# Optimization experiments

Measured on AMD Instinct MI355X. Metric: run time of the kernel, lower is better.

Reference implementation:

```python
import jax, jax.numpy as jnp
import numpy as np

NUM_SEGMENTS = 4
SIZE_SEG = 2  # sqrt(num_segments)


def conv2d_same(x, w, b):
    # x: [B,C,H,W], w: [O,I,3,3], padding=1, stride=1
    y = jax.lax.conv_general_dilated(
        x, w, window_strides=(1, 1), padding=((1, 1), (1, 1)),
        dimension_numbers=("NCHW", "OIHW", "NCHW"))
    return y + b[None, :, None, None]


def setup_inputs() -> dict:
    key = jax.random.key(0)
    k1, k2, k3, k4, k5 = jax.random.split(key, 5)
    B, C, H, W = 4, 64, 512, 512
    x = jax.random.normal(k1, (B, C, H, W), dtype=jnp.float32)
    # Conv params (kaiming-ish small scale)
    local_w = jax.random.normal(k2, (NUM_SEGMENTS, NUM_SEGMENTS, 3, 3), dtype=jnp.float32) * 0.1
    local_b = jax.random.normal(k3, (NUM_SEGMENTS,), dtype=jnp.float32) * 0.01
    global_w = jax.random.normal(k4, (1, 2, 3, 3), dtype=jnp.float32) * 0.1
    global_b = jax.random.normal(k5, (1,), dtype=jnp.float32) * 0.01
    return {"x": x, "local_w": local_w, "local_b": local_b,
            "global_w": global_w, "global_b": global_b}


def local_attention(x, w, b):
    B, C, H, W = x.shape
    s = SIZE_SEG
    Hs, Ws = H // s, W // s
    # L2 norm over channel dim, keepdim -> [B,1,H,W]
    l2 = jnp.sqrt(jnp.sum(x * x, axis=1, keepdims=True))
    # Split into s*s spatial tiles, stacked on channel dim in (i,j) row-major order
    # [B,1,H,W] -> [B,s,Hs,s,Ws] -> [B,s,s,Hs,Ws] -> [B,s*s,Hs,Ws]
    tiles = l2[:, 0].reshape(B, s, Hs, s, Ws).transpose(0, 1, 3, 2, 4).reshape(B, s * s, Hs, Ws)
    out = jax.nn.sigmoid(conv2d_same(tiles, w, b))  # [B, s*s, Hs, Ws]
    # torch: chunk along ch, cat along dim2, view(l2.shape) == flat row-major reshape
    return out.reshape(B, 1, H, W)


def global_attention(x, w, b):
    max_out = jnp.max(x, axis=1, keepdims=True)
    mean_out = jnp.mean(x, axis=1, keepdims=True)
    cat = jnp.concatenate([max_out, mean_out], axis=1)  # [B,2,H,W]
    return jax.nn.sigmoid(jax.nn.relu(conv2d_same(cat, w, b)))


def reference(x, local_w, local_b, global_w, global_b):
    return local_attention(x, local_w, local_b) + global_attention(x, global_w, global_b)
```

## Files before the change

kernel.cpp:

```cpp
#include <hip/hip_runtime.h>
#include <math.h>

#define HH 512
#define WW 512
#define HW (HH * WW)
#define CCH 64
#define BB 4

typedef float    f4 __attribute__((ext_vector_type(4)));
typedef _Float16 h2 __attribute__((ext_vector_type(2)));
typedef _Float16 h4 __attribute__((ext_vector_type(4)));
typedef _Float16 h8 __attribute__((ext_vector_type(8)));

__global__ __launch_bounds__(256) void reduce_k(const float* __restrict__ x,
                                                _Float16* __restrict__ l2p,
                                                h2* __restrict__ mmp) {
    int tid = blockIdx.x * 256 + threadIdx.x;
    int b  = tid >> 16;
    int p4 = tid & 65535;

    const f4* xb = reinterpret_cast<const f4*>(x)
                 + (size_t)b * CCH * (HW / 4) + p4;

    f4 ss = {0.f, 0.f, 0.f, 0.f};
    f4 sm = {0.f, 0.f, 0.f, 0.f};
    f4 mx = {-INFINITY, -INFINITY, -INFINITY, -INFINITY};

#pragma unroll 16
    for (int c = 0; c < CCH; ++c) {
        f4 v = xb[(size_t)c * (HW / 4)];
        ss += v * v;
        sm += v;
        mx.x = fmaxf(mx.x, v.x);
        mx.y = fmaxf(mx.y, v.y);
        mx.z = fmaxf(mx.z, v.z);
        mx.w = fmaxf(mx.w, v.w);
    }

    size_t o4 = (size_t)b * (HW / 4) + p4;
    const float inv = 1.0f / 64.0f;
    h8 mm = { (_Float16)mx.x, (_Float16)(sm.x * inv),
              (_Float16)mx.y, (_Float16)(sm.y * inv),
              (_Float16)mx.z, (_Float16)(sm.z * inv),
              (_Float16)mx.w, (_Float16)(sm.w * inv) };
    h4 l2v = { (_Float16)sqrtf(ss.x), (_Float16)sqrtf(ss.y),
               (_Float16)sqrtf(ss.z), (_Float16)sqrtf(ss.w) };
    reinterpret_cast<h8*>(mmp)[o4] = mm;
    reinterpret_cast<h4*>(l2p)[o4] = l2v;
}

__global__ __launch_bounds__(256) void attn_k(const _Float16* __restrict__ l2p,
                                              const h2* __restrict__ mmp,
                                              const float* __restrict__ lw,
                                              const float* __restrict__ lb,
                                              const float* __restrict__ gw,
                                              const float* __restrict__ gb,
                                              float* __restrict__ out) {
    __shared__ float s_lw[144];
    __shared__ float s_lb[4];
    __shared__ float s_gw[18];
    __shared__ float s_gb;

    int t = threadIdx.x;
    if (t < 144) s_lw[t] = lw[t];
    if (t < 4)   s_lb[t] = lb[t];
    if (t < 18)  s_gw[t] = gw[t];
    if (t == 0)  s_gb = gb[0];
    __syncthreads();

    int idx4 = blockIdx.x * 256 + t;
    int b  = idx4 >> 16;
    int p4 = idx4 & 65535;
    int h  = p4 >> 7;
    int w0 = (p4 & 127) << 2;

    const _Float16* l2b = l2p + ((size_t)b << 18);
    const h2*       mmb = mmp + ((size_t)b << 18);

    float g0 = s_gb, g1 = s_gb, g2 = s_gb, g3 = s_gb;
#pragma unroll
    for (int dh = -1; dh <= 1; ++dh) {
        int hh = h + dh;
        if ((unsigned)hh >= (unsigned)HH) continue;
        const h2* row = mmb + hh * WW + w0;
        h8 v = *reinterpret_cast<const h8*>(row);
        float m6[6], a6[6];
        if (w0 > 0) { h2 e = row[-1]; m6[0] = (float)e.x; a6[0] = (float)e.y; }
        else        { m6[0] = 0.f;    a6[0] = 0.f; }
        m6[1] = (float)v[0]; a6[1] = (float)v[1];
        m6[2] = (float)v[2]; a6[2] = (float)v[3];
        m6[3] = (float)v[4]; a6[3] = (float)v[5];
        m6[4] = (float)v[6]; a6[4] = (float)v[7];
        if (w0 < WW - 4) { h2 e = row[4]; m6[5] = (float)e.x; a6[5] = (float)e.y; }
        else             { m6[5] = 0.f;   a6[5] = 0.f; }
#pragma unroll
        for (int k = 0; k < 3; ++k) {
            float wmk = s_gw[(dh + 1) * 3 + k];
            float wak = s_gw[9 + (dh + 1) * 3 + k];
            g0 = fmaf(m6[0 + k], wmk, fmaf(a6[0 + k], wak, g0));
            g1 = fmaf(m6[1 + k], wmk, fmaf(a6[1 + k], wak, g1));
            g2 = fmaf(m6[2 + k], wmk, fmaf(a6[2 + k], wak, g2));
            g3 = fmaf(m6[3 + k], wmk, fmaf(a6[3 + k], wak, g3));
        }
    }

    int c   = h >> 7;
    int hs  = ((h & 127) << 1) | (w0 >> 8);
    int ws0 = w0 & 255;

    float la0 = s_lb[c], la1 = la0, la2 = la0, la3 = la0;
#pragma unroll
    for (int i = 0; i < 4; ++i) {
        const _Float16* base = l2b + (i >> 1) * (256 * WW) + (i & 1) * 256;
        const float* wi = s_lw + c * 36 + i * 9;
#pragma unroll
        for (int dh = -1; dh <= 1; ++dh) {
            int y = hs + dh;
            if ((unsigned)y >= 256u) continue;
            const _Float16* row = base + y * WW + ws0;
            h4 v = *reinterpret_cast<const h4*>(row);
            float v6[6];
            v6[0] = (ws0 > 0)   ? (float)row[-1] : 0.f;
            v6[1] = (float)v[0]; v6[2] = (float)v[1];
            v6[3] = (float)v[2]; v6[4] = (float)v[3];
            v6[5] = (ws0 < 252) ? (float)row[4]  : 0.f;
#pragma unroll
            for (int k = 0; k < 3; ++k) {
                float wk = wi[(dh + 1) * 3 + k];
                la0 = fmaf(v6[0 + k], wk, la0);
                la1 = fmaf(v6[1 + k], wk, la1);
                la2 = fmaf(v6[2 + k], wk, la2);
                la3 = fmaf(v6[3 + k], wk, la3);
            }
        }
    }

    f4 o;
    o.x = 1.f / (1.f + __expf(-la0)) + 1.f / (1.f + __expf(-fmaxf(g0, 0.f)));
    o.y = 1.f / (1.f + __expf(-la1)) + 1.f / (1.f + __expf(-fmaxf(g1, 0.f)));
    o.z = 1.f / (1.f + __expf(-la2)) + 1.f / (1.f + __expf(-fmaxf(g2, 0.f)));
    o.w = 1.f / (1.f + __expf(-la3)) + 1.f / (1.f + __expf(-fmaxf(g3, 0.f)));
    __builtin_nontemporal_store(o, reinterpret_cast<f4*>(out) + idx4);
}

extern "C" void kernel_launch(void* const* d_in, const int* in_sizes, int n_in,
                              void* d_out, int out_size, void* d_ws, size_t ws_size,
                              hipStream_t stream) {
    const float* x  = (const float*)d_in[0];
    const float* lw = (const float*)d_in[1];
    const float* lb = (const float*)d_in[2];
    const float* gw = (const float*)d_in[3];
    const float* gb = (const float*)d_in[4];
    float* out = (float*)d_out;

    h2*       mmp = (h2*)d_ws;
    _Float16* l2p = (_Float16*)((char*)d_ws + (size_t)BB * HW * sizeof(h2));

    int n1 = BB * HW / 4;
    reduce_k<<<n1 / 256, 256, 0, stream>>>(x, l2p, mmp);

    int n2 = BB * HW / 4;
    attn_k<<<n2 / 256, 256, 0, stream>>>(l2p, mmp, lw, lb, gw, gb, out);
}
```

Before: 58.23 us.

## Process eight pixels per thread and stagger channel start across blocks

Both kernels now handle eight pixels per thread instead of four, which halves the thread count and widens loads and stores to 8-element vectors. This amortises halo loads and index math in the attention kernel. The reduction kernel also rotates its starting channel by block index so concurrent blocks hit different channel planes, spreading DRAM traffic across channels. In exchange each thread uses more registers, fewer waves are in flight, and each thread's two float4 loads per channel are still strided.

```diff
diff --git a/kernel.cpp b/kernel.cpp
--- a/kernel.cpp
+++ b/kernel.cpp
@@ -9,44 +9,60 @@
 
 typedef float    f4 __attribute__((ext_vector_type(4)));
 typedef _Float16 h2 __attribute__((ext_vector_type(2)));
-typedef _Float16 h4 __attribute__((ext_vector_type(4)));
 typedef _Float16 h8 __attribute__((ext_vector_type(8)));
 
 __global__ __launch_bounds__(256) void reduce_k(const float* __restrict__ x,
                                                 _Float16* __restrict__ l2p,
                                                 h2* __restrict__ mmp) {
     int tid = blockIdx.x * 256 + threadIdx.x;
-    int b  = tid >> 16;
-    int p4 = tid & 65535;
+    int b  = tid >> 15;
+    int p8 = tid & 32767;
 
     const f4* xb = reinterpret_cast<const f4*>(x)
-                 + (size_t)b * CCH * (HW / 4) + p4;
+                 + (size_t)b * CCH * (HW / 4) + (size_t)p8 * 2;
 
-    f4 ss = {0.f, 0.f, 0.f, 0.f};
-    f4 sm = {0.f, 0.f, 0.f, 0.f};
-    f4 mx = {-INFINITY, -INFINITY, -INFINITY, -INFINITY};
+    f4 ss0 = {0.f, 0.f, 0.f, 0.f}, ss1 = ss0;
+    f4 sm0 = ss0, sm1 = ss0;
+    f4 mx0 = {-INFINITY, -INFINITY, -INFINITY, -INFINITY}, mx1 = mx0;
 
-#pragma unroll 16
-    for (int c = 0; c < CCH; ++c) {
-        f4 v = xb[(size_t)c * (HW / 4)];
-        ss += v * v;
-        sm += v;
-        mx.x = fmaxf(mx.x, v.x);
-        mx.y = fmaxf(mx.y, v.y);
-        mx.z = fmaxf(mx.z, v.z);
-        mx.w = fmaxf(mx.w, v.w);
+#define RED_BODY(c)                                                   \
+    {                                                                 \
+        const f4* p = xb + (size_t)(c) * (HW / 4);                    \
+        f4 v0 = p[0];                                                 \
+        f4 v1 = p[1];                                                 \
+        ss0 += v0 * v0;  ss1 += v1 * v1;                              \
+        sm0 += v0;       sm1 += v1;                                   \
+        mx0.x = fmaxf(mx0.x, v0.x); mx0.y = fmaxf(mx0.y, v0.y);       \
+        mx0.z = fmaxf(mx0.z, v0.z); mx0.w = fmaxf(mx0.w, v0.w);       \
+        mx1.x = fmaxf(mx1.x, v1.x); mx1.y = fmaxf(mx1.y, v1.y);       \
+        mx1.z = fmaxf(mx1.z, v1.z); mx1.w = fmaxf(mx1.w, v1.w);       \
     }
 
-    size_t o4 = (size_t)b * (HW / 4) + p4;
+    int c0 = (blockIdx.x & 7) * 8;
+#pragma unroll 8
+    for (int c = c0; c < CCH; ++c) RED_BODY(c)
+#pragma unroll 8
+    for (int c = 0; c < c0; ++c) RED_BODY(c)
+#undef RED_BODY
+
     const float inv = 1.0f / 64.0f;
-    h8 mm = { (_Float16)mx.x, (_Float16)(sm.x * inv),
-              (_Float16)mx.y, (_Float16)(sm.y * inv),
-              (_Float16)mx.z, (_Float16)(sm.z * inv),
-              (_Float16)mx.w, (_Float16)(sm.w * inv) };
-    h4 l2v = { (_Float16)sqrtf(ss.x), (_Float16)sqrtf(ss.y),
-               (_Float16)sqrtf(ss.z), (_Float16)sqrtf(ss.w) };
-    reinterpret_cast<h8*>(mmp)[o4] = mm;
-    reinterpret_cast<h4*>(l2p)[o4] = l2v;
+    h8 mmA = { (_Float16)mx0.x, (_Float16)(sm0.x * inv),
+               (_Float16)mx0.y, (_Float16)(sm0.y * inv),
+               (_Float16)mx0.z, (_Float16)(sm0.z * inv),
+               (_Float16)mx0.w, (_Float16)(sm0.w * inv) };
+    h8 mmB = { (_Float16)mx1.x, (_Float16)(sm1.x * inv),
+               (_Float16)mx1.y, (_Float16)(sm1.y * inv),
+               (_Float16)mx1.z, (_Float16)(sm1.z * inv),
+               (_Float16)mx1.w, (_Float16)(sm1.w * inv) };
+    h8 l2v = { (_Float16)sqrtf(ss0.x), (_Float16)sqrtf(ss0.y),
+               (_Float16)sqrtf(ss0.z), (_Float16)sqrtf(ss0.w),
+               (_Float16)sqrtf(ss1.x), (_Float16)sqrtf(ss1.y),
+               (_Float16)sqrtf(ss1.z), (_Float16)sqrtf(ss1.w) };
+
+    size_t o8 = (size_t)b * (HW / 8) + p8;
+    reinterpret_cast<h8*>(mmp)[o8 * 2]     = mmA;
+    reinterpret_cast<h8*>(mmp)[o8 * 2 + 1] = mmB;
+    reinterpret_cast<h8*>(l2p)[o8]         = l2v;
 }
 
 __global__ __launch_bounds__(256) void attn_k(const _Float16* __restrict__ l2p,
@@ -68,39 +84,42 @@
     if (t == 0)  s_gb = gb[0];
     __syncthreads();
 
-    int idx4 = blockIdx.x * 256 + t;
-    int b  = idx4 >> 16;
-    int p4 = idx4 & 65535;
-    int h  = p4 >> 7;
-    int w0 = (p4 & 127) << 2;
+    int idx8 = blockIdx.x * 256 + t;
+    int b  = idx8 >> 15;
+    int p8 = idx8 & 32767;
+    int h  = p8 >> 6;
+    int w0 = (p8 & 63) << 3;
 
     const _Float16* l2b = l2p + ((size_t)b << 18);
     const h2*       mmb = mmp + ((size_t)b << 18);
 
-    float g0 = s_gb, g1 = s_gb, g2 = s_gb, g3 = s_gb;
+    float g[8];
+#pragma unroll
+    for (int j = 0; j < 8; ++j) g[j] = s_gb;
 #pragma unroll
     for (int dh = -1; dh <= 1; ++dh) {
         int hh = h + dh;
         if ((unsigned)hh >= (unsigned)HH) continue;
         const h2* row = mmb + hh * WW + w0;
-        h8 v = *reinterpret_cast<const h8*>(row);
-        float m6[6], a6[6];
-        if (w0 > 0) { h2 e = row[-1]; m6[0] = (float)e.x; a6[0] = (float)e.y; }
-        else        { m6[0] = 0.f;    a6[0] = 0.f; }
-        m6[1] = (float)v[0]; a6[1] = (float)v[1];
-        m6[2] = (float)v[2]; a6[2] = (float)v[3];
-        m6[3] = (float)v[4]; a6[3] = (float)v[5];
-        m6[4] = (float)v[6]; a6[4] = (float)v[7];
-        if (w0 < WW - 4) { h2 e = row[4]; m6[5] = (float)e.x; a6[5] = (float)e.y; }
-        else             { m6[5] = 0.f;   a6[5] = 0.f; }
+        h8 vA = *reinterpret_cast<const h8*>(row);
+        h8 vB = *reinterpret_cast<const h8*>(row + 4);
+        float m10[10], a10[10];
+        if (w0 > 0) { h2 e = row[-1]; m10[0] = (float)e.x; a10[0] = (float)e.y; }
+        else        { m10[0] = 0.f;   a10[0] = 0.f; }
+#pragma unroll
+        for (int j = 0; j < 4; ++j) {
+            m10[1 + j] = (float)vA[2 * j];  a10[1 + j] = (float)vA[2 * j + 1];
+            m10[5 + j] = (float)vB[2 * j];  a10[5 + j] = (float)vB[2 * j + 1];
+        }
+        if (w0 < WW - 8) { h2 e = row[8]; m10[9] = (float)e.x; a10[9] = (float)e.y; }
+        else             { m10[9] = 0.f;  a10[9] = 0.f; }
 #pragma unroll
         for (int k = 0; k < 3; ++k) {
             float wmk = s_gw[(dh + 1) * 3 + k];
             float wak = s_gw[9 + (dh + 1) * 3 + k];
-            g0 = fmaf(m6[0 + k], wmk, fmaf(a6[0 + k], wak, g0));
-            g1 = fmaf(m6[1 + k], wmk, fmaf(a6[1 + k], wak, g1));
-            g2 = fmaf(m6[2 + k], wmk, fmaf(a6[2 + k], wak, g2));
-            g3 = fmaf(m6[3 + k], wmk, fmaf(a6[3 + k], wak, g3));
+#pragma unroll
+            for (int j = 0; j < 8; ++j)
+                g[j] = fmaf(m10[j + k], wmk, fmaf(a10[j + k], wak, g[j]));
         }
     }
 
@@ -108,7 +127,9 @@
     int hs  = ((h & 127) << 1) | (w0 >> 8);
     int ws0 = w0 & 255;
 
-    float la0 = s_lb[c], la1 = la0, la2 = la0, la3 = la0;
+    float la[8];
+#pragma unroll
+    for (int j = 0; j < 8; ++j) la[j] = s_lb[c];
 #pragma unroll
     for (int i = 0; i < 4; ++i) {
         const _Float16* base = l2b + (i >> 1) * (256 * WW) + (i & 1) * 256;
@@ -118,29 +139,32 @@
             int y = hs + dh;
             if ((unsigned)y >= 256u) continue;
             const _Float16* row = base + y * WW + ws0;
-            h4 v = *reinterpret_cast<const h4*>(row);
-            float v6[6];
-            v6[0] = (ws0 > 0)   ? (float)row[-1] : 0.f;
-            v6[1] = (float)v[0]; v6[2] = (float)v[1];
-            v6[3] = (float)v[2]; v6[4] = (float)v[3];
-            v6[5] = (ws0 < 252) ? (float)row[4]  : 0.f;
+            h8 v = *reinterpret_cast<const h8*>(row);
+            float v10[10];
+            v10[0] = (ws0 > 0)   ? (float)row[-1] : 0.f;
+#pragma unroll
+            for (int j = 0; j < 8; ++j) v10[1 + j] = (float)v[j];
+            v10[9] = (ws0 < 248) ? (float)row[8]  : 0.f;
 #pragma unroll
             for (int k = 0; k < 3; ++k) {
                 float wk = wi[(dh + 1) * 3 + k];
-                la0 = fmaf(v6[0 + k], wk, la0);
-                la1 = fmaf(v6[1 + k], wk, la1);
-                la2 = fmaf(v6[2 + k], wk, la2);
-                la3 = fmaf(v6[3 + k], wk, la3);
+#pragma unroll
+                for (int j = 0; j < 8; ++j)
+                    la[j] = fmaf(v10[j + k], wk, la[j]);
             }
         }
     }
 
-    f4 o;
-    o.x = 1.f / (1.f + __expf(-la0)) + 1.f / (1.f + __expf(-fmaxf(g0, 0.f)));
-    o.y = 1.f / (1.f + __expf(-la1)) + 1.f / (1.f + __expf(-fmaxf(g1, 0.f)));
-    o.z = 1.f / (1.f + __expf(-la2)) + 1.f / (1.f + __expf(-fmaxf(g2, 0.f)));
-    o.w = 1.f / (1.f + __expf(-la3)) + 1.f / (1.f + __expf(-fmaxf(g3, 0.f)));
-    __builtin_nontemporal_store(o, reinterpret_cast<f4*>(out) + idx4);
+    f4 oA, oB;
+#pragma unroll
+    for (int j = 0; j < 4; ++j) {
+        oA[j] = 1.f / (1.f + __expf(-la[j]))
+              + 1.f / (1.f + __expf(-fmaxf(g[j], 0.f)));
+        oB[j] = 1.f / (1.f + __expf(-la[4 + j]))
+              + 1.f / (1.f + __expf(-fmaxf(g[4 + j], 0.f)));
+    }
+    __builtin_nontemporal_store(oA, reinterpret_cast<f4*>(out) + idx8 * 2);
+    __builtin_nontemporal_store(oB, reinterpret_cast<f4*>(out) + idx8 * 2 + 1);
 }
 
 extern "C" void kernel_launch(void* const* d_in, const int* in_sizes, int n_in,
@@ -156,9 +180,9 @@
     h2*       mmp = (h2*)d_ws;
     _Float16* l2p = (_Float16*)((char*)d_ws + (size_t)BB * HW * sizeof(h2));
 
-    int n1 = BB * HW / 4;
+    int n1 = BB * HW / 8;
     reduce_k<<<n1 / 256, 256, 0, stream>>>(x, l2p, mmp);
 
-    int n2 = BB * HW / 4;
+    int n2 = BB * HW / 8;
     attn_k<<<n2 / 256, 256, 0, stream>>>(l2p, mmp, lw, lb, gw, gb, out);
 }
```

New measurement: 58.42 us. Within noise of the previous version (+0.3%).
